# Performance work log

Measured on AMD Instinct MI355X. Metric: run time of the kernel, lower is better.

The kernel has to match this reference:

```python
import jax, jax.numpy as jnp
import numpy as np

DIM = 16  # scale_size[0] * scale_size[1]
SCALE = DIM ** -0.5


def setup_inputs() -> dict:
    key = jax.random.key(0)
    k1, k2 = jax.random.split(key)
    x = jax.random.normal(k1, (16, 256, 256, 64), dtype=jnp.float32)
    # torch Linear(dim, 2*dim, bias=False): weight shape [32, 16]
    w_qkv = jax.random.normal(k2, (32, 16), dtype=jnp.float32) * (DIM ** -0.5)
    return {"x": x, "w_qkv": w_qkv}


def reference(x, w_qkv):
    B, H, W, C = x.shape
    sh, sw = 4, 4  # scale_size
    # permute to (b, c, h, w) then adaptive avg pool to (4, 4)
    xp = jnp.transpose(x, (0, 3, 1, 2))  # [B, C, H, W]
    pooled = xp.reshape(B, C, sh, H // sh, sw, W // sw).mean(axis=(3, 5))  # [B, C, 4, 4]
    tokens = pooled.reshape(B, C, DIM)  # [B, C, 16]
    # to_qkv: Linear with weight [2*dim, dim] -> x @ W^T, then chunk
    qk = jnp.einsum('bcn,dn->bcd', tokens, w_qkv)  # [B, C, 32]
    q, k = qk[..., :DIM], qk[..., DIM:]  # each [B, C, 16]
    dots = jnp.einsum('bin,bjn->bij', q, k) * SCALE  # [B, C, C]
    attn = jax.nn.softmax(dots, axis=-1)  # [B, C, C]
    out = jnp.einsum('bhwc,btc->bhwt', x, attn)  # [B, H, W, C]
    return jax.nn.gelu(out, approximate=False)
```

## Files before the change

### kernel.cpp

```cpp
#include <hip/hip_runtime.h>
#include <math.h>
#include <cstddef>

#define BB   16
#define HH   256
#define WW   256
#define CC   64
#define NTOK 16
#define NDIM 16
#define HALF_B 8

#define PART_FLOATS (BB * NTOK * 16 * CC)
#define FRAG_USHORT_PER_B (8 * 64 * 8)

typedef short s16x8 __attribute__((ext_vector_type(8)));
typedef float f32x4 __attribute__((ext_vector_type(4)));

__device__ __forceinline__ unsigned short f2bf_rne(float f) {
    unsigned int u = __float_as_uint(f);
    return (unsigned short)((u + 0x7fffu + ((u >> 16) & 1u)) >> 16);
}

__global__ __launch_bounds__(256) void pool_partial(const float* __restrict__ x,
                                                    float* __restrict__ part,
                                                    int b0) {
    const int blk = blockIdx.x;
    const int rc  = blk & 15;
    const int n   = (blk >> 4) & 15;
    const int b   = b0 + (blk >> 8);
    const int ph  = n >> 2, pw = n & 3;
    const int t   = threadIdx.x;
    const int c4  = (t & 15) << 2;
    const int sub = t >> 4;

    const int h0 = ph * 64 + rc * 4;
    const int w0 = pw * 64;
    const float* xb = x + (((size_t)b * HH + h0) * WW + w0) * CC;

    float4 s = make_float4(0.f, 0.f, 0.f, 0.f);
#pragma unroll
    for (int k = 0; k < 16; ++k) {
        const int pos = sub + (k << 4);
        const int row = pos >> 6;
        const int col = pos & 63;
        const float4 v = *(const float4*)(xb + ((size_t)row * WW + col) * CC + c4);
        s.x += v.x; s.y += v.y; s.z += v.z; s.w += v.w;
    }

    __shared__ float lds[16 * 64];
    lds[sub * 64 + c4 + 0] = s.x;
    lds[sub * 64 + c4 + 1] = s.y;
    lds[sub * 64 + c4 + 2] = s.z;
    lds[sub * 64 + c4 + 3] = s.w;
    __syncthreads();

    if (t < 64) {
        float acc = 0.f;
#pragma unroll
        for (int ss = 0; ss < 16; ++ss) acc += lds[ss * 64 + t];
        part[(((size_t)b * NTOK + n) * 16 + rc) * CC + t] = acc;
    }
}

__global__ __launch_bounds__(256) void attn_kernel(const float* __restrict__ part,
                                                   const float* __restrict__ w_qkv,
                                                   unsigned short* __restrict__ fragw,
                                                   int b0) {
    const int b = b0 + blockIdx.x;
    const int t = threadIdx.x;

    __shared__ float tok[CC * NDIM];
    __shared__ float ql [CC * NDIM];
    __shared__ float kl [CC * NDIM];
    __shared__ float dl [CC * CC];
    __shared__ float rs [CC];

    const float* pb = part + (size_t)b * NTOK * 16 * CC;

    {
        const int n  = t >> 4;
        const int cq = t & 15;
        float4 a = make_float4(0.f, 0.f, 0.f, 0.f);
#pragma unroll
        for (int rc = 0; rc < 16; ++rc) {
            const float4 v = *(const float4*)(pb + ((size_t)n * 16 + rc) * CC + cq * 4);
            a.x += v.x; a.y += v.y; a.z += v.z; a.w += v.w;
        }
        tok[(cq * 4 + 0) * NDIM + n] = a.x * (1.0f / 4096.0f);
        tok[(cq * 4 + 1) * NDIM + n] = a.y * (1.0f / 4096.0f);
        tok[(cq * 4 + 2) * NDIM + n] = a.z * (1.0f / 4096.0f);
        tok[(cq * 4 + 3) * NDIM + n] = a.w * (1.0f / 4096.0f);
    }
    __syncthreads();

    for (int idx = t; idx < CC * 32; idx += 256) {
        const int c = idx >> 5, d = idx & 31;
        float a = 0.f;
#pragma unroll
        for (int n = 0; n < NDIM; ++n) a += tok[c * NDIM + n] * w_qkv[d * NDIM + n];
        if (d < 16) ql[c * NDIM + d] = a;
        else        kl[c * NDIM + (d - 16)] = a;
    }
    __syncthreads();

    for (int idx = t; idx < CC * CC; idx += 256) {
        const int i = idx >> 6, j = idx & 63;
        float a = 0.f;
#pragma unroll
        for (int n = 0; n < NDIM; ++n) a += ql[i * NDIM + n] * kl[j * NDIM + n];
        dl[idx] = a * 0.25f;
    }
    __syncthreads();

    if (t < CC) {
        float m = -1e30f;
        for (int j = 0; j < CC; ++j) m = fmaxf(m, dl[t * CC + j]);
        float ssum = 0.f;
        for (int j = 0; j < CC; ++j) {
            const float e = expf(dl[t * CC + j] - m);
            dl[t * CC + j] = e;
            ssum += e;
        }
        rs[t] = 1.0f / ssum;
    }
    __syncthreads();

    for (int idx = t; idx < 512; idx += 256) {
        const int tt   = idx >> 3;
        const int oct  = idx & 7;
        const int ks   = oct >> 2;
        const int g    = oct & 3;
        const int slot = (tt >> 4) * 2 + ks;
        const int lanei = (tt & 15) + g * 16;
        const float rr = rs[tt];
        s16x8 hi;
#pragma unroll
        for (int j = 0; j < 8; ++j)
            hi[j] = (short)f2bf_rne(dl[tt * CC + oct * 8 + j] * rr);
        s16x8* dst = (s16x8*)fragw + ((size_t)b * 8 + slot) * 64;
        dst[lanei] = hi;
    }
}

__device__ __forceinline__ float gelu_fast(float v) {
    const float u = v * v;
    const float z = v * fmaf(0.07135482f, u, 1.59576912f);
    const float e = exp2f(z * -1.44269504f);
    return v * __builtin_amdgcn_rcpf(e + 1.0f);
}

__device__ __forceinline__ s16x8 pack8(const float4 a, const float4 b) {
    union { unsigned int u[4]; s16x8 v; } r;
    asm("v_cvt_pk_bf16_f32 %0, %1, %2" : "=v"(r.u[0]) : "v"(a.x), "v"(a.y));
    asm("v_cvt_pk_bf16_f32 %0, %1, %2" : "=v"(r.u[1]) : "v"(a.z), "v"(a.w));
    asm("v_cvt_pk_bf16_f32 %0, %1, %2" : "=v"(r.u[2]) : "v"(b.x), "v"(b.y));
    asm("v_cvt_pk_bf16_f32 %0, %1, %2" : "=v"(r.u[3]) : "v"(b.z), "v"(b.w));
    return r.v;
}

__global__ __launch_bounds__(256) void out_mfma(const float* __restrict__ x,
                                                const unsigned short* __restrict__ frag,
                                                float* __restrict__ out,
                                                int b0) {
    const int tid  = threadIdx.x;
    const int lane = tid & 63;
    const int wv   = tid >> 6;
    const int blk  = b0 * 256 + (int)blockIdx.x;
    const int b    = blk >> 8;
    const int row  = lane & 15;
    const int g    = lane >> 4;

    const size_t pix0 = (size_t)blk * 256 + wv * 64;
    const float* xb = x + (pix0 + row) * CC + g * 8;

    float4 a0 = *(const float4*)(xb);
    float4 a1 = *(const float4*)(xb + 4);
    float4 a2 = *(const float4*)(xb + 32);
    float4 a3 = *(const float4*)(xb + 36);

    const s16x8* fb = (const s16x8*)(frag + (size_t)b * FRAG_USHORT_PER_B);
    s16x8 bf[8];
#pragma unroll
    for (int s = 0; s < 8; ++s) bf[s] = fb[s * 64 + lane];

    const float* x1 = xb + 16 * CC;
    float4 b0v = *(const float4*)(x1);
    float4 b1v = *(const float4*)(x1 + 4);
    float4 b2v = *(const float4*)(x1 + 32);
    float4 b3v = *(const float4*)(x1 + 36);

    float* ob = out + (pix0 + (g << 2)) * CC + row;

#define TCOLS(RB, AH0, AH1)                                                     \
    _Pragma("unroll")                                                           \
    for (int tcol = 0; tcol < 4; ++tcol) {                                      \
        f32x4 acc = {0.f, 0.f, 0.f, 0.f};                                       \
        acc = __builtin_amdgcn_mfma_f32_16x16x32_bf16(AH0, bf[tcol * 2], acc, 0, 0, 0);     \
        acc = __builtin_amdgcn_mfma_f32_16x16x32_bf16(AH1, bf[tcol * 2 + 1], acc, 0, 0, 0); \
        float* o = ob + (size_t)(RB) * 16 * CC + tcol * 16;                     \
        _Pragma("unroll")                                                       \
        for (int r = 0; r < 4; ++r) o[(size_t)r * CC] = gelu_fast(acc[r]);      \
    }

    {
        const s16x8 ah0 = pack8(a0, a1);
        const s16x8 ah1 = pack8(a2, a3);
        const float* nx = xb + 32 * CC;
        a0 = *(const float4*)(nx);
        a1 = *(const float4*)(nx + 4);
        a2 = *(const float4*)(nx + 32);
        a3 = *(const float4*)(nx + 36);
        TCOLS(0, ah0, ah1)
    }
    {
        const s16x8 ah0 = pack8(b0v, b1v);
        const s16x8 ah1 = pack8(b2v, b3v);
        const float* nx = xb + 48 * CC;
        b0v = *(const float4*)(nx);
        b1v = *(const float4*)(nx + 4);
        b2v = *(const float4*)(nx + 32);
        b3v = *(const float4*)(nx + 36);
        TCOLS(1, ah0, ah1)
    }
    {
        const s16x8 ah0 = pack8(a0, a1);
        const s16x8 ah1 = pack8(a2, a3);
        TCOLS(2, ah0, ah1)
    }
    {
        const s16x8 ah0 = pack8(b0v, b1v);
        const s16x8 ah1 = pack8(b2v, b3v);
        TCOLS(3, ah0, ah1)
    }
#undef TCOLS
}

extern "C" void kernel_launch(void* const* d_in, const int* in_sizes, int n_in,
                              void* d_out, int out_size, void* d_ws, size_t ws_size,
                              hipStream_t stream) {
    const float* x     = (const float*)d_in[0];
    const float* w_qkv = (const float*)d_in[1];
    float* out   = (float*)d_out;
    float* part  = (float*)d_ws;
    unsigned short* frag = (unsigned short*)(part + PART_FLOATS);

    for (int h = 0; h < 2; ++h) {
        const int b0 = h * HALF_B;
        pool_partial<<<HALF_B * NTOK * 16, 256, 0, stream>>>(x, part, b0);
        attn_kernel<<<HALF_B, 256, 0, stream>>>(part, w_qkv, frag, b0);
        out_mfma<<<HALF_B * 256, 256, 0, stream>>>(x, frag, out, b0);
    }
}
```

Baseline: 515.1 us.

## Process whole batch in one pass and transpose MFMA output for vector stores

Removes the two half-batch passes and launches pooling, attention and output kernels once each over all 16 batches. The output MFMA swaps its operands so each lane holds four consecutive output channels, which lets every result tile be written with one 16-byte store instead of four scattered scalar stores. This cuts launch count and store instructions. The trade-off is that x (about 268 MB) no longer splits into halves small enough to stay cache-resident between the pooling read and the output read, which may raise DRAM traffic.

```diff
diff --git a/kernel.cpp b/kernel.cpp
--- a/kernel.cpp
+++ b/kernel.cpp
@@ -8,7 +8,6 @@
 #define CC   64
 #define NTOK 16
 #define NDIM 16
-#define HALF_B 8
 
 #define PART_FLOATS (BB * NTOK * 16 * CC)
 #define FRAG_USHORT_PER_B (8 * 64 * 8)
@@ -22,12 +21,11 @@
 }
 
 __global__ __launch_bounds__(256) void pool_partial(const float* __restrict__ x,
-                                                    float* __restrict__ part,
-                                                    int b0) {
+                                                    float* __restrict__ part) {
     const int blk = blockIdx.x;
     const int rc  = blk & 15;
     const int n   = (blk >> 4) & 15;
-    const int b   = b0 + (blk >> 8);
+    const int b   = blk >> 8;
     const int ph  = n >> 2, pw = n & 3;
     const int t   = threadIdx.x;
     const int c4  = (t & 15) << 2;
@@ -64,9 +62,8 @@
 
 __global__ __launch_bounds__(256) void attn_kernel(const float* __restrict__ part,
                                                    const float* __restrict__ w_qkv,
-                                                   unsigned short* __restrict__ fragw,
-                                                   int b0) {
-    const int b = b0 + blockIdx.x;
+                                                   unsigned short* __restrict__ fragw) {
+    const int b = blockIdx.x;
     const int t = threadIdx.x;
 
     __shared__ float tok[CC * NDIM];
@@ -160,12 +157,11 @@
 
 __global__ __launch_bounds__(256) void out_mfma(const float* __restrict__ x,
                                                 const unsigned short* __restrict__ frag,
-                                                float* __restrict__ out,
-                                                int b0) {
+                                                float* __restrict__ out) {
     const int tid  = threadIdx.x;
     const int lane = tid & 63;
     const int wv   = tid >> 6;
-    const int blk  = b0 * 256 + (int)blockIdx.x;
+    const int blk  = blockIdx.x;
     const int b    = blk >> 8;
     const int row  = lane & 15;
     const int g    = lane >> 4;
@@ -189,48 +185,49 @@
     float4 b2v = *(const float4*)(x1 + 32);
     float4 b3v = *(const float4*)(x1 + 36);
 
-    float* ob = out + (pix0 + (g << 2)) * CC + row;
-
-#define TCOLS(RB, AH0, AH1)                                                     \
-    _Pragma("unroll")                                                           \
-    for (int tcol = 0; tcol < 4; ++tcol) {                                      \
-        f32x4 acc = {0.f, 0.f, 0.f, 0.f};                                       \
-        acc = __builtin_amdgcn_mfma_f32_16x16x32_bf16(AH0, bf[tcol * 2], acc, 0, 0, 0);     \
-        acc = __builtin_amdgcn_mfma_f32_16x16x32_bf16(AH1, bf[tcol * 2 + 1], acc, 0, 0, 0); \
-        float* o = ob + (size_t)(RB) * 16 * CC + tcol * 16;                     \
-        _Pragma("unroll")                                                       \
-        for (int r = 0; r < 4; ++r) o[(size_t)r * CC] = gelu_fast(acc[r]);      \
-    }
-
-    {
-        const s16x8 ah0 = pack8(a0, a1);
-        const s16x8 ah1 = pack8(a2, a3);
+    float* ob = out + (pix0 + row) * CC + (g << 2);
+
+#define TCOLS(PT, XH0, XH1)                                                      \
+    _Pragma("unroll")                                                            \
+    for (int tt = 0; tt < 4; ++tt) {                                             \
+        f32x4 acc = {0.f, 0.f, 0.f, 0.f};                                        \
+        acc = __builtin_amdgcn_mfma_f32_16x16x32_bf16(bf[tt * 2], XH0, acc, 0, 0, 0);     \
+        acc = __builtin_amdgcn_mfma_f32_16x16x32_bf16(bf[tt * 2 + 1], XH1, acc, 0, 0, 0); \
+        f32x4 gv;                                                                \
+        gv.x = gelu_fast(acc.x); gv.y = gelu_fast(acc.y);                        \
+        gv.z = gelu_fast(acc.z); gv.w = gelu_fast(acc.w);                        \
+        *(f32x4*)(ob + (size_t)(PT) * 16 * CC + tt * 16) = gv;                   \
+    }
+
+    {
+        const s16x8 xh0 = pack8(a0, a1);
+        const s16x8 xh1 = pack8(a2, a3);
         const float* nx = xb + 32 * CC;
         a0 = *(const float4*)(nx);
         a1 = *(const float4*)(nx + 4);
         a2 = *(const float4*)(nx + 32);
         a3 = *(const float4*)(nx + 36);
-        TCOLS(0, ah0, ah1)
-    }
-    {
-        const s16x8 ah0 = pack8(b0v, b1v);
-        const s16x8 ah1 = pack8(b2v, b3v);
+        TCOLS(0, xh0, xh1)
+    }
+    {
+        const s16x8 xh0 = pack8(b0v, b1v);
+        const s16x8 xh1 = pack8(b2v, b3v);
         const float* nx = xb + 48 * CC;
         b0v = *(const float4*)(nx);
         b1v = *(const float4*)(nx + 4);
         b2v = *(const float4*)(nx + 32);
         b3v = *(const float4*)(nx + 36);
-        TCOLS(1, ah0, ah1)
-    }
-    {
-        const s16x8 ah0 = pack8(a0, a1);
-        const s16x8 ah1 = pack8(a2, a3);
-        TCOLS(2, ah0, ah1)
-    }
-    {
-        const s16x8 ah0 = pack8(b0v, b1v);
-        const s16x8 ah1 = pack8(b2v, b3v);
-        TCOLS(3, ah0, ah1)
+        TCOLS(1, xh0, xh1)
+    }
+    {
+        const s16x8 xh0 = pack8(a0, a1);
+        const s16x8 xh1 = pack8(a2, a3);
+        TCOLS(2, xh0, xh1)
+    }
+    {
+        const s16x8 xh0 = pack8(b0v, b1v);
+        const s16x8 xh1 = pack8(b2v, b3v);
+        TCOLS(3, xh0, xh1)
     }
 #undef TCOLS
 }
@@ -244,10 +241,7 @@
     float* part  = (float*)d_ws;
     unsigned short* frag = (unsigned short*)(part + PART_FLOATS);
 
-    for (int h = 0; h < 2; ++h) {
-        const int b0 = h * HALF_B;
-        pool_partial<<<HALF_B * NTOK * 16, 256, 0, stream>>>(x, part, b0);
-        attn_kernel<<<HALF_B, 256, 0, stream>>>(part, w_qkv, frag, b0);
-        out_mfma<<<HALF_B * 256, 256, 0, stream>>>(x, frag, out, b0);
-    }
-}
+    pool_partial<<<BB * NTOK * 16, 256, 0, stream>>>(x, part);
+    attn_kernel<<<BB, 256, 0, stream>>>(part, w_qkv, frag);
+    out_mfma<<<BB * 256, 256, 0, stream>>>(x, frag, out);
+}
```

Result: no change. 515.6 us (+0.1%).
